# Performance work log

Hardware: AMD Instinct MI355X
Metric: run time of the kernel (lower is better)

The kernel has to match this reference:

```python
import jax, jax.numpy as jnp
import numpy as np

B, S, D, H = 8, 2048, 1024, 1024

def setup_inputs() -> dict:
    key = jax.random.key(0)
    ks = jax.random.split(key, 7)
    scale_in = 1.0 / np.sqrt(D)
    return {
        "x": jax.random.normal(ks[0], (B, S, D), dtype=jnp.float32),
        "Wq": jax.random.normal(ks[1], (D, H), dtype=jnp.float32) * scale_in,
        "bq": jnp.zeros((H,), dtype=jnp.float32),
        "Wk": jax.random.normal(ks[2], (D, H), dtype=jnp.float32) * scale_in,
        "bk": jnp.zeros((H,), dtype=jnp.float32),
        "Wv": jax.random.normal(ks[3], (D, H), dtype=jnp.float32) * scale_in,
        "bv": jnp.zeros((H,), dtype=jnp.float32),
    }

def reference(x, Wq, bq, Wk, bk, Wv, bv):
    # projections: [B,S,D] @ [D,H] -> [B,S,H]
    q = jnp.einsum("bsd,dh->bsh", x, Wq) + bq
    k = jnp.einsum("bsd,dh->bsh", x, Wk) + bk
    v = jnp.einsum("bsd,dh->bsh", x, Wv) + bv
    scale = 1.0 / jnp.sqrt(jnp.asarray(q.shape[-1], q.dtype))
    scores = jnp.einsum("bqh,bkh->bqk", q, k) * scale  # [B,S,S]
    attention_weights = jax.nn.softmax(scores, axis=-1)
    weighted_sum = jnp.einsum("bqk,bkh->bqh", attention_weights, v)
    return (weighted_sum, attention_weights)
```

## Files before the change

### kernel.cpp

```cpp
#include <hip/hip_runtime.h>
#include <hip/hip_fp16.h>


typedef _Float16 half8_t __attribute__((ext_vector_type(8)));
typedef _Float16 half4_t __attribute__((ext_vector_type(4)));
typedef float    floatx4 __attribute__((ext_vector_type(4)));

__device__ __forceinline__ void async_copy16(void* lds, const void* gptr) {
    __builtin_amdgcn_global_load_lds(
        (const __attribute__((address_space(1))) void*)gptr,
        (__attribute__((address_space(3))) void*)lds,
        16, 0, 0);
}

__global__ __launch_bounds__(256)
void cvt_f32_f16(const float* __restrict__ in, _Float16* __restrict__ out, long long n4) {
    long long i = (long long)blockIdx.x * 256 + threadIdx.x;
    if (i < n4) {
        float4 v = ((const float4*)in)[i];
        half4_t h = {(_Float16)v.x, (_Float16)v.y, (_Float16)v.z, (_Float16)v.w};
        *(half4_t*)&out[i * 4] = h;
    }
}

__global__ __launch_bounds__(256)
void transpose_cvt(const float* __restrict__ in, _Float16* __restrict__ out, int R, int C) {
    __shared__ float tile[32][33];
    int c0 = blockIdx.x * 32, r0 = blockIdx.y * 32;
    int tx = threadIdx.x & 31, ty = threadIdx.x >> 5;
#pragma unroll
    for (int i = 0; i < 32; i += 8)
        tile[ty + i][tx] = in[(long long)(r0 + ty + i) * C + c0 + tx];
    __syncthreads();
#pragma unroll
    for (int i = 0; i < 32; i += 8)
        out[(long long)(c0 + ty + i) * R + r0 + tx] = (_Float16)tile[tx][ty + i];
}

__global__ __launch_bounds__(256)
void transpose_h(const _Float16* __restrict__ in, _Float16* __restrict__ out, int R, int C) {
    long long z = blockIdx.z;
    in  += z * (long long)R * C;
    out += z * (long long)R * C;
    __shared__ _Float16 tile[32][33];
    int c0 = blockIdx.x * 32, r0 = blockIdx.y * 32;
    int tx = threadIdx.x & 31, ty = threadIdx.x >> 5;
#pragma unroll
    for (int i = 0; i < 32; i += 8)
        tile[ty + i][tx] = in[(long long)(r0 + ty + i) * C + c0 + tx];
    __syncthreads();
#pragma unroll
    for (int i = 0; i < 32; i += 8)
        out[(long long)(c0 + ty + i) * R + r0 + tx] = tile[tx][ty + i];
}

#define STAGE(gptr, bufB, opOff, KK, KT) {                                    \
    const _Float16* _s = (gptr) + (KT) * 64 + (KK) * 32;                      \
    char* _d = sm + (bufB) + (opOff) + (KK) * 16384 + stW;                    \
    async_copy16(_d,        _s);                                              \
    async_copy16(_d + 8192, _s + (long long)128 * K); }

#define LOAD_A(I0, KK, CB) {                                                  \
    const char* _p = sm + (CB) + (KK) * 16384 + offA0;                        \
    aq[0] = *(const half8_t*)(_p + ((I0) + 0) * 1024);                        \
    aq[1] = *(const half8_t*)(_p + ((I0) + 1) * 1024);                        \
    aq[2] = *(const half8_t*)(_p + ((I0) + 2) * 1024);                        \
    aq[3] = *(const half8_t*)(_p + ((I0) + 3) * 1024); }

#define LOAD_B(KK, CB) {                                                      \
    const char* _p = sm + (CB) + 32768 + (KK) * 16384 + offB0;                \
    bq[0] = *(const half8_t*)(_p + 0);                                        \
    bq[1] = *(const half8_t*)(_p + 1024);                                     \
    bq[2] = *(const half8_t*)(_p + 2048);                                     \
    bq[3] = *(const half8_t*)(_p + 3072); }

#define MFMA16(I0)                                                            \
    __builtin_amdgcn_s_barrier();                                             \
    __builtin_amdgcn_s_setprio(1);                                            \
    _Pragma("unroll") for (int _i = 0; _i < 4; ++_i)                          \
    _Pragma("unroll") for (int _j = 0; _j < 4; ++_j)                          \
        acc[(I0) + _i][_j] = __builtin_amdgcn_mfma_f32_16x16x32_f16(          \
            aq[_i], bq[_j], acc[(I0) + _i][_j], 0, 0, 0);                     \
    __builtin_amdgcn_s_setprio(0);                                            \
    __builtin_amdgcn_s_barrier();

template <bool OUT_HALF>
__global__ __launch_bounds__(512, 2)
void gemm256(const _Float16* __restrict__ A, const _Float16* __restrict__ Bt,
             float* __restrict__ Cf, _Float16* __restrict__ Ch,
             int N, int K,
             long long sA, long long sB, long long sC,
             float scale, const float* __restrict__ bias)
{
    __shared__ __align__(16) char smem[131072];
    char* sm = (char*)smem;

    const int z = blockIdx.z;
    const _Float16* Ao = A  + (long long)z * sA;
    const _Float16* Bo = Bt + (long long)z * sB;

    const int gx = gridDim.x, nwg = gx * gridDim.y;
    int wg = blockIdx.y * gx + blockIdx.x;
    {
        int q = nwg >> 3, r = nwg & 7;
        int xcd = wg & 7, pos = wg >> 3;
        wg = (xcd < r ? xcd * (q + 1) : r * (q + 1) + (xcd - r) * q) + pos;
    }
    const int tileN = wg % gx;
    const int tileM = wg / gx;

    const int t    = threadIdx.x;
    const int lane = t & 63;
    const int w    = t >> 6;
    const int fr   = lane & 15;
    const int g    = lane >> 4;

    const int swz   = ((g ^ ((fr >> 1) & 3)) << 4);
    const int offA0 = (((w >> 2) * 128 + fr) << 6) + swz;
    const int offB0 = (((w & 3) * 64 + fr) << 6) + swz;

    const int srow = w * 16 + (lane >> 2);
    const int scol = (((lane & 3) ^ ((lane >> 3) & 3)) << 3);
    const _Float16* gA = Ao + (long long)(tileM * 256 + srow) * K + scol;
    const _Float16* gB = Bo + (long long)(tileN * 256 + srow) * K + scol;
    const int stW = w * 1024;

    floatx4 acc[8][4];
#pragma unroll
    for (int i = 0; i < 8; ++i)
#pragma unroll
        for (int j = 0; j < 4; ++j)
            acc[i][j] = (floatx4){0.f, 0.f, 0.f, 0.f};

    half8_t aq[4], bq[4];

    const int NT = K >> 6;

    STAGE(gA, 0, 0,     0, 0);
    STAGE(gB, 0, 32768, 0, 0);
    STAGE(gA, 0, 0,     1, 0);
    STAGE(gB, 0, 32768, 1, 0);
    asm volatile("s_waitcnt vmcnt(4)");
    __builtin_amdgcn_s_barrier();

    for (int kt = 0; kt < NT; ++kt) {
        const int cB = (kt & 1) << 16;
        const int nB = cB ^ 65536;
        const bool more = (kt + 1) < NT;

        LOAD_A(0, 0, cB); LOAD_B(0, cB);
        if (more) STAGE(gA, nB, 0, 0, kt + 1);
        MFMA16(0);

        LOAD_A(4, 0, cB);
        if (more) { STAGE(gB, nB, 32768, 0, kt + 1); asm volatile("s_waitcnt vmcnt(4)"); }
        else      { asm volatile("s_waitcnt vmcnt(0)"); }
        MFMA16(4);

        LOAD_A(0, 1, cB); LOAD_B(1, cB);
        if (more) STAGE(gA, nB, 0, 1, kt + 1);
        MFMA16(0);

        LOAD_A(4, 1, cB);
        if (more) { STAGE(gB, nB, 32768, 1, kt + 1); asm volatile("s_waitcnt vmcnt(4)"); }
        MFMA16(4);
        __builtin_amdgcn_sched_barrier(0);
    }

    const int orow = tileM * 256 + (w >> 2) * 128 + g * 4;
    const int ocol = tileN * 256 + (w & 3) * 64 + fr;
#pragma unroll
    for (int j = 0; j < 4; ++j) {
        const int col = ocol + j * 16;
        const float bv = bias ? bias[col] : 0.f;
#pragma unroll
        for (int i = 0; i < 8; ++i) {
#pragma unroll
            for (int r = 0; r < 4; ++r) {
                const int row = orow + i * 16 + r;
                const long long off = (long long)z * sC + (long long)row * N + col;
                const float val = acc[i][j][r] * scale + bv;
                if (OUT_HALF) Ch[off] = (_Float16)val;
                else          Cf[off] = val;
            }
        }
    }
}

__global__ __launch_bounds__(256)
void softmax_kernel(float* __restrict__ attn, _Float16* __restrict__ Ph, int S) {
    const long long row = blockIdx.x;
    float*     rp = attn + row * S;
    _Float16*  pp = Ph   + row * S;
    const int t = threadIdx.x;
    const int lane = t & 63, wave = t >> 6;

    float4 v0 = ((const float4*)rp)[t * 2];
    float4 v1 = ((const float4*)rp)[t * 2 + 1];
    float e[8] = {v0.x, v0.y, v0.z, v0.w, v1.x, v1.y, v1.z, v1.w};

    float m = e[0];
#pragma unroll
    for (int i = 1; i < 8; ++i) m = fmaxf(m, e[i]);
#pragma unroll
    for (int off = 32; off > 0; off >>= 1) m = fmaxf(m, __shfl_xor(m, off, 64));

    __shared__ float redm[4];
    __shared__ float reds[4];
    if (lane == 0) redm[wave] = m;
    __syncthreads();
    m = fmaxf(fmaxf(redm[0], redm[1]), fmaxf(redm[2], redm[3]));

    float s = 0.f;
#pragma unroll
    for (int i = 0; i < 8; ++i) { e[i] = __expf(e[i] - m); s += e[i]; }
#pragma unroll
    for (int off = 32; off > 0; off >>= 1) s += __shfl_xor(s, off, 64);
    if (lane == 0) reds[wave] = s;
    __syncthreads();
    s = reds[0] + reds[1] + reds[2] + reds[3];
    const float inv = 1.f / s;

    float4 o0 = {e[0] * inv, e[1] * inv, e[2] * inv, e[3] * inv};
    float4 o1 = {e[4] * inv, e[5] * inv, e[6] * inv, e[7] * inv};
    ((float4*)rp)[t * 2]     = o0;
    ((float4*)rp)[t * 2 + 1] = o1;

    half8_t h;
#pragma unroll
    for (int i = 0; i < 8; ++i) h[i] = (_Float16)(e[i] * inv);
    *(half8_t*)&pp[t * 8] = h;
}

extern "C" void kernel_launch(void* const* d_in, const int* in_sizes, int n_in,
                              void* d_out, int out_size, void* d_ws, size_t ws_size,
                              hipStream_t stream)
{
    const int B = 8, S = 2048, D = 1024, H = 1024;
    const float* x  = (const float*)d_in[0];
    const float* Wq = (const float*)d_in[1];
    const float* bq = (const float*)d_in[2];
    const float* Wk = (const float*)d_in[3];
    const float* bk = (const float*)d_in[4];
    const float* Wv = (const float*)d_in[5];
    const float* bv = (const float*)d_in[6];

    float* outO = (float*)d_out;
    float* outP = (float*)d_out + (long long)B * S * H;

    char* ws = (char*)d_ws;
    const long long SZ_X  = (long long)B * S * D * 2;
    const long long SZ_W  = (long long)D * H * 2;
    _Float16* xh  = (_Float16*)(ws);
    _Float16* wqt = (_Float16*)(ws + SZ_X);
    _Float16* wkt = (_Float16*)(ws + SZ_X + SZ_W);
    _Float16* wvt = (_Float16*)(ws + SZ_X + 2 * SZ_W);
    _Float16* qh  = (_Float16*)(ws + SZ_X + 3 * SZ_W);
    _Float16* kh  = (_Float16*)(ws + SZ_X + 3 * SZ_W + SZ_X);
    _Float16* vh  = (_Float16*)(ws + SZ_X + 3 * SZ_W + 2 * SZ_X);
    _Float16* vt  = (_Float16*)(ws + SZ_X + 3 * SZ_W + 3 * SZ_X);
    _Float16* ph  = qh;

    {
        long long n4 = (long long)B * S * D / 4;
        cvt_f32_f16<<<(unsigned)((n4 + 255) / 256), 256, 0, stream>>>(x, xh, n4);
    }
    {
        dim3 g(H / 32, D / 32);
        transpose_cvt<<<g, 256, 0, stream>>>(Wq, wqt, D, H);
        transpose_cvt<<<g, 256, 0, stream>>>(Wk, wkt, D, H);
        transpose_cvt<<<g, 256, 0, stream>>>(Wv, wvt, D, H);
    }
    {
        dim3 g(H / 256, (B * S) / 256, 1);
        gemm256<true><<<g, 512, 0, stream>>>(xh, wqt, nullptr, qh, H, D, 0, 0, 0, 1.f, bq);
        gemm256<true><<<g, 512, 0, stream>>>(xh, wkt, nullptr, kh, H, D, 0, 0, 0, 1.f, bk);
        gemm256<true><<<g, 512, 0, stream>>>(xh, wvt, nullptr, vh, H, D, 0, 0, 0, 1.f, bv);
    }
    {
        dim3 g(H / 32, S / 32, B);
        transpose_h<<<g, 256, 0, stream>>>(vh, vt, S, H);
    }
    {
        dim3 g(S / 256, S / 256, B);
        gemm256<false><<<g, 512, 0, stream>>>(qh, kh, outP, nullptr, S, H,
                                              (long long)S * H, (long long)S * H,
                                              (long long)S * S, 0.03125f, nullptr);
    }
    softmax_kernel<<<B * S, 256, 0, stream>>>(outP, ph, S);
    {
        dim3 g(H / 256, S / 256, B);
        gemm256<false><<<g, 512, 0, stream>>>(ph, vt, outO, nullptr, H, S,
                                              (long long)S * S, (long long)H * S,
                                              (long long)S * H, 1.f, nullptr);
    }
}
```

Before: 623.3 us.

## Fuse Q/K/V projections into one GEMM and vectorize the V transpose

Concatenates the transposed Wq/Wk/Wv into one [3H, D] weight and runs a single GEMM that produces an interleaved QKV buffer, selecting the bias by column. Downstream GEMMs and softmax now take explicit leading dimensions so they read Q, K and V in place, and P is written over the Q/K columns. The V transpose becomes a 64x64 tile kernel with 16-byte vector loads and stores. The aim is fewer launches, a larger grid that fills the GPU better, better reuse of x, and cheaper transposes. The cost is strided access into a wider buffer.

```diff
diff --git a/kernel.cpp b/kernel.cpp
--- a/kernel.cpp
+++ b/kernel.cpp
@@ -38,27 +38,41 @@
 }
 
 __global__ __launch_bounds__(256)
-void transpose_h(const _Float16* __restrict__ in, _Float16* __restrict__ out, int R, int C) {
-    long long z = blockIdx.z;
-    in  += z * (long long)R * C;
-    out += z * (long long)R * C;
-    __shared__ _Float16 tile[32][33];
-    int c0 = blockIdx.x * 32, r0 = blockIdx.y * 32;
-    int tx = threadIdx.x & 31, ty = threadIdx.x >> 5;
-#pragma unroll
-    for (int i = 0; i < 32; i += 8)
-        tile[ty + i][tx] = in[(long long)(r0 + ty + i) * C + c0 + tx];
+void transpose_h64(const _Float16* __restrict__ in, long long zin, int ldin,
+                   _Float16* __restrict__ out, long long zout, int ldout) {
+    const long long z = blockIdx.z;
+    in  += z * zin;
+    out += z * zout;
+    __shared__ _Float16 tile[64][66];
+    const int t  = threadIdx.x;
+    const int r0 = blockIdx.y * 64, c0 = blockIdx.x * 64;
+    const int col8 = (t & 7) * 8;
+    const int row  = t >> 3;
+#pragma unroll
+    for (int p = 0; p < 2; ++p) {
+        const int r = row + p * 32;
+        half8_t v = *(const half8_t*)&in[(long long)(r0 + r) * ldin + c0 + col8];
+#pragma unroll
+        for (int i = 0; i < 8; ++i) tile[r][col8 + i] = v[i];
+    }
     __syncthreads();
-#pragma unroll
-    for (int i = 0; i < 32; i += 8)
-        out[(long long)(c0 + ty + i) * R + r0 + tx] = tile[tx][ty + i];
-}
-
-#define STAGE(gptr, bufB, opOff, KK, KT) {                                    \
+    const int c  = t >> 3;
+    const int rb = (t & 7) * 8;
+#pragma unroll
+    for (int p = 0; p < 2; ++p) {
+        const int cc = c + p * 32;
+        half8_t v;
+#pragma unroll
+        for (int i = 0; i < 8; ++i) v[i] = tile[rb + i][cc];
+        *(half8_t*)&out[(long long)(c0 + cc) * ldout + r0 + rb] = v;
+    }
+}
+
+#define STAGE(gptr, LD, bufB, opOff, KK, KT) {                                \
     const _Float16* _s = (gptr) + (KT) * 64 + (KK) * 32;                      \
     char* _d = sm + (bufB) + (opOff) + (KK) * 16384 + stW;                    \
     async_copy16(_d,        _s);                                              \
-    async_copy16(_d + 8192, _s + (long long)128 * K); }
+    async_copy16(_d + 8192, _s + (long long)128 * (LD)); }
 
 #define LOAD_A(I0, KK, CB) {                                                  \
     const char* _p = sm + (CB) + (KK) * 16384 + offA0;                        \
@@ -88,9 +102,11 @@
 __global__ __launch_bounds__(512, 2)
 void gemm256(const _Float16* __restrict__ A, const _Float16* __restrict__ Bt,
              float* __restrict__ Cf, _Float16* __restrict__ Ch,
-             int N, int K,
+             int K, int ldA, int ldB, int ldC,
              long long sA, long long sB, long long sC,
-             float scale, const float* __restrict__ bias)
+             float scale,
+             const float* __restrict__ b0, const float* __restrict__ b1,
+             const float* __restrict__ b2)
 {
     __shared__ __align__(16) char smem[131072];
     char* sm = (char*)smem;
@@ -121,8 +137,8 @@
 
     const int srow = w * 16 + (lane >> 2);
     const int scol = (((lane & 3) ^ ((lane >> 3) & 3)) << 3);
-    const _Float16* gA = Ao + (long long)(tileM * 256 + srow) * K + scol;
-    const _Float16* gB = Bo + (long long)(tileN * 256 + srow) * K + scol;
+    const _Float16* gA = Ao + (long long)(tileM * 256 + srow) * ldA + scol;
+    const _Float16* gB = Bo + (long long)(tileN * 256 + srow) * ldB + scol;
     const int stW = w * 1024;
 
     floatx4 acc[8][4];
@@ -136,10 +152,10 @@
 
     const int NT = K >> 6;
 
-    STAGE(gA, 0, 0,     0, 0);
-    STAGE(gB, 0, 32768, 0, 0);
-    STAGE(gA, 0, 0,     1, 0);
-    STAGE(gB, 0, 32768, 1, 0);
+    STAGE(gA, ldA, 0, 0,     0, 0);
+    STAGE(gB, ldB, 0, 32768, 0, 0);
+    STAGE(gA, ldA, 0, 0,     1, 0);
+    STAGE(gB, ldB, 0, 32768, 1, 0);
     asm volatile("s_waitcnt vmcnt(4)");
     __builtin_amdgcn_s_barrier();
 
@@ -149,20 +165,20 @@
         const bool more = (kt + 1) < NT;
 
         LOAD_A(0, 0, cB); LOAD_B(0, cB);
-        if (more) STAGE(gA, nB, 0, 0, kt + 1);
+        if (more) STAGE(gA, ldA, nB, 0, 0, kt + 1);
         MFMA16(0);
 
         LOAD_A(4, 0, cB);
-        if (more) { STAGE(gB, nB, 32768, 0, kt + 1); asm volatile("s_waitcnt vmcnt(4)"); }
+        if (more) { STAGE(gB, ldB, nB, 32768, 0, kt + 1); asm volatile("s_waitcnt vmcnt(4)"); }
         else      { asm volatile("s_waitcnt vmcnt(0)"); }
         MFMA16(4);
 
         LOAD_A(0, 1, cB); LOAD_B(1, cB);
-        if (more) STAGE(gA, nB, 0, 1, kt + 1);
+        if (more) STAGE(gA, ldA, nB, 0, 1, kt + 1);
         MFMA16(0);
 
         LOAD_A(4, 1, cB);
-        if (more) { STAGE(gB, nB, 32768, 1, kt + 1); asm volatile("s_waitcnt vmcnt(4)"); }
+        if (more) { STAGE(gB, ldB, nB, 32768, 1, kt + 1); asm volatile("s_waitcnt vmcnt(4)"); }
         MFMA16(4);
         __builtin_amdgcn_sched_barrier(0);
     }
@@ -172,13 +188,14 @@
 #pragma unroll
     for (int j = 0; j < 4; ++j) {
         const int col = ocol + j * 16;
-        const float bv = bias ? bias[col] : 0.f;
+        float bv = 0.f;
+        if (b0) bv = col < 1024 ? b0[col] : (col < 2048 ? b1[col - 1024] : b2[col - 2048]);
 #pragma unroll
         for (int i = 0; i < 8; ++i) {
 #pragma unroll
             for (int r = 0; r < 4; ++r) {
                 const int row = orow + i * 16 + r;
-                const long long off = (long long)z * sC + (long long)row * N + col;
+                const long long off = (long long)z * sC + (long long)row * ldC + col;
                 const float val = acc[i][j][r] * scale + bv;
                 if (OUT_HALF) Ch[off] = (_Float16)val;
                 else          Cf[off] = val;
@@ -188,10 +205,11 @@
 }
 
 __global__ __launch_bounds__(256)
-void softmax_kernel(float* __restrict__ attn, _Float16* __restrict__ Ph, int S) {
+void softmax_kernel(float* __restrict__ attn, _Float16* __restrict__ Ph,
+                    int S, int ldP) {
     const long long row = blockIdx.x;
     float*     rp = attn + row * S;
-    _Float16*  pp = Ph   + row * S;
+    _Float16*  pp = Ph   + row * (long long)ldP;
     const int t = threadIdx.x;
     const int lane = t & 63, wave = t >> 6;
 
@@ -237,6 +255,7 @@
                               hipStream_t stream)
 {
     const int B = 8, S = 2048, D = 1024, H = 1024;
+    const int N3 = 3 * H;
     const float* x  = (const float*)d_in[0];
     const float* Wq = (const float*)d_in[1];
     const float* bq = (const float*)d_in[2];
@@ -249,17 +268,13 @@
     float* outP = (float*)d_out + (long long)B * S * H;
 
     char* ws = (char*)d_ws;
-    const long long SZ_X  = (long long)B * S * D * 2;
-    const long long SZ_W  = (long long)D * H * 2;
-    _Float16* xh  = (_Float16*)(ws);
-    _Float16* wqt = (_Float16*)(ws + SZ_X);
-    _Float16* wkt = (_Float16*)(ws + SZ_X + SZ_W);
-    _Float16* wvt = (_Float16*)(ws + SZ_X + 2 * SZ_W);
-    _Float16* qh  = (_Float16*)(ws + SZ_X + 3 * SZ_W);
-    _Float16* kh  = (_Float16*)(ws + SZ_X + 3 * SZ_W + SZ_X);
-    _Float16* vh  = (_Float16*)(ws + SZ_X + 3 * SZ_W + 2 * SZ_X);
-    _Float16* vt  = (_Float16*)(ws + SZ_X + 3 * SZ_W + 3 * SZ_X);
-    _Float16* ph  = qh;
+    const long long SZ_XH   = (long long)B * S * D * 2;
+    const long long SZ_W3   = (long long)N3 * D * 2;
+    const long long SZ_QKV  = (long long)B * S * N3 * 2;
+    _Float16* xh    = (_Float16*)(ws);
+    _Float16* wqkvt = (_Float16*)(ws + SZ_XH);
+    _Float16* qkv   = (_Float16*)(ws + SZ_XH + SZ_W3);
+    _Float16* vt    = (_Float16*)(ws + SZ_XH + SZ_W3 + SZ_QKV);
 
     {
         long long n4 = (long long)B * S * D / 4;
@@ -267,31 +282,35 @@
     }
     {
         dim3 g(H / 32, D / 32);
-        transpose_cvt<<<g, 256, 0, stream>>>(Wq, wqt, D, H);
-        transpose_cvt<<<g, 256, 0, stream>>>(Wk, wkt, D, H);
-        transpose_cvt<<<g, 256, 0, stream>>>(Wv, wvt, D, H);
-    }
-    {
-        dim3 g(H / 256, (B * S) / 256, 1);
-        gemm256<true><<<g, 512, 0, stream>>>(xh, wqt, nullptr, qh, H, D, 0, 0, 0, 1.f, bq);
-        gemm256<true><<<g, 512, 0, stream>>>(xh, wkt, nullptr, kh, H, D, 0, 0, 0, 1.f, bk);
-        gemm256<true><<<g, 512, 0, stream>>>(xh, wvt, nullptr, vh, H, D, 0, 0, 0, 1.f, bv);
-    }
-    {
-        dim3 g(H / 32, S / 32, B);
-        transpose_h<<<g, 256, 0, stream>>>(vh, vt, S, H);
+        transpose_cvt<<<g, 256, 0, stream>>>(Wq, wqkvt,             D, H);
+        transpose_cvt<<<g, 256, 0, stream>>>(Wk, wqkvt + (long long)H * D,     D, H);
+        transpose_cvt<<<g, 256, 0, stream>>>(Wv, wqkvt + (long long)2 * H * D, D, H);
+    }
+    {
+        dim3 g(N3 / 256, (B * S) / 256, 1);
+        gemm256<true><<<g, 512, 0, stream>>>(xh, wqkvt, nullptr, qkv,
+                                             D, D, D, N3, 0, 0, 0, 1.f, bq, bk, bv);
+    }
+    {
+        dim3 g(H / 64, S / 64, B);
+        transpose_h64<<<g, 256, 0, stream>>>(qkv + 2 * H, (long long)S * N3, N3,
+                                             vt, (long long)H * S, S);
     }
     {
         dim3 g(S / 256, S / 256, B);
-        gemm256<false><<<g, 512, 0, stream>>>(qh, kh, outP, nullptr, S, H,
-                                              (long long)S * H, (long long)S * H,
-                                              (long long)S * S, 0.03125f, nullptr);
-    }
-    softmax_kernel<<<B * S, 256, 0, stream>>>(outP, ph, S);
+        gemm256<false><<<g, 512, 0, stream>>>(qkv, qkv + H, outP, nullptr,
+                                              D, N3, N3, S,
+                                              (long long)S * N3, (long long)S * N3,
+                                              (long long)S * S, 0.03125f,
+                                              nullptr, nullptr, nullptr);
+    }
+    softmax_kernel<<<B * S, 256, 0, stream>>>(outP, qkv, S, N3);
     {
         dim3 g(H / 256, S / 256, B);
-        gemm256<false><<<g, 512, 0, stream>>>(ph, vt, outO, nullptr, H, S,
-                                              (long long)S * S, (long long)H * S,
-                                              (long long)S * H, 1.f, nullptr);
-    }
-}
+        gemm256<false><<<g, 512, 0, stream>>>(qkv, vt, outO, nullptr,
+                                              S, N3, S, H,
+                                              (long long)S * N3, (long long)H * S,
+                                              (long long)S * H, 1.f,
+                                              nullptr, nullptr, nullptr);
+    }
+}
```

Result: faster. 601.8 us (-3.5%).
